# Performance work log

Measured on AMD Instinct MI355X. Metric: run time of the kernel, lower is better.

## Reference

```python
import jax, jax.numpy as jnp
import numpy as np

HEADS = 16
DIM_HEAD = 64
HEIGHT = 16
KERNEL = 5
DILATION = 1
ALPHA = 32 ** 2


def stable_softmax(t, axis=-1, alpha=ALPHA):
    t = t / alpha
    t = t - jax.lax.stop_gradient(jnp.max(t, axis=axis, keepdims=True))
    return jax.nn.softmax(t * alpha, axis=axis)


def setup_inputs() -> dict:
    key = jax.random.key(0)
    ks = jax.random.split(key, 5)
    b, n, dim = 4, 4097, 1024
    inner = HEADS * DIM_HEAD
    x = jax.random.normal(ks[0], (b, n, dim), dtype=jnp.float32)
    w_qkv = jax.random.normal(ks[1], (dim, 3 * inner), dtype=jnp.float32) * (dim ** -0.5)
    w_out = jax.random.normal(ks[2], (inner, dim), dtype=jnp.float32) * (inner ** -0.5)
    b_out = jax.random.normal(ks[3], (dim,), dtype=jnp.float32) * 0.02
    w_th = jax.random.normal(ks[4], (HEADS, HEADS), dtype=jnp.float32) * (HEADS ** -0.5)
    return {"x": x, "w_qkv": w_qkv, "w_out": w_out, "b_out": b_out, "w_th": w_th}


def reference(x, w_qkv, w_out, b_out, w_th):
    b, n, dim = x.shape
    h, d = HEADS, DIM_HEAD
    height, K, dil = HEIGHT, KERNEL, DILATION
    pad = dil * (K - 1) // 2
    scale = d ** -0.5
    kernel_numel = K * height

    # pad (n-1) non-BOS tokens to a multiple of height (static shapes)
    seq_pad = (-(n - 1)) % height
    xp = jnp.pad(x, ((0, 0), (0, seq_pad), (0, 0))) if seq_pad > 0 else x

    qkv = xp @ w_qkv  # [b, np, 3*inner]
    q, k, v = jnp.split(qkv, 3, axis=-1)

    if n == 1:  # bos-only path
        return v @ w_out + b_out

    out_bos = v[:, :1]  # [b, 1, inner]

    def to_heads(t):
        return t.reshape(b, -1, h, d).transpose(0, 2, 1, 3)  # [b,h,np,d]

    q, k, v = map(to_heads, (q, k, v))
    q = q * scale

    k_bos, k = k[:, :, 0], k[:, :, 1:]
    v_bos, v = v[:, :, 0], v[:, :, 1:]
    q = q[:, :, 1:]

    X = q.shape[2] // height  # number of timesteps

    # k, v as 2D grids [b,h,X,height,d]; unfold local windows along timestep axis
    k = k.reshape(b, h, X, height, d)
    v = v.reshape(b, h, X, height, d)
    kp = jnp.pad(k, ((0, 0), (0, 0), (pad, pad), (0, 0), (0, 0)))
    vp = jnp.pad(v, ((0, 0), (0, 0), (pad, pad), (0, 0), (0, 0)))
    idx = jnp.arange(X)[:, None] + jnp.arange(K)[None, :] * dil  # [X, K]
    kw = kp[:, :, idx].reshape(b, h, X, kernel_numel, d)  # [b,h,X,K*height,d]
    vw = vp[:, :, idx].reshape(b, h, X, kernel_numel, d)

    # prepend BOS key/value to every window
    kb = jnp.broadcast_to(k_bos[:, :, None, None, :], (b, h, X, 1, d))
    vb = jnp.broadcast_to(v_bos[:, :, None, None, :], (b, h, X, 1, d))
    kw = jnp.concatenate([kb, kw], axis=3)  # [b,h,X,1+kn,d]
    vw = jnp.concatenate([vb, vw], axis=3)

    qw = q.reshape(b, h, X, height, d)  # [b,h,X,height,d]
    sim = jnp.einsum('bhnid,bhnjd->bhnij', qw, kw)  # [b,h,X,height,1+kn]

    # causal mask over unfolded windows (BOS column never masked)
    seq_len = X * height
    q_range = jnp.arange(seq_len).reshape(X, height)
    k_range = jnp.pad(jnp.arange(seq_len).reshape(X, height), ((pad, pad), (0, 0)),
                      constant_values=seq_len)
    kr = k_range[idx].reshape(X, kernel_numel)  # [X, kn]
    mask = q_range[:, :, None] < kr[:, None, :]  # [X, height, kn]
    mask = jnp.pad(mask, ((0, 0), (0, 0), (1, 0)), constant_values=False)

    mask_value = -jnp.finfo(sim.dtype).max
    sim = jnp.where(mask[None, None], mask_value, sim)

    attn = stable_softmax(sim, axis=-1)
    # talking heads: 1x1x1 Conv3d over head channels == head mixing matmul
    attn = jnp.einsum('gh,bhnij->bgnij', w_th, attn)

    out = jnp.einsum('bhnij,bhnjd->bhnid', attn, vw)  # [b,h,X,height,d]
    out = out.transpose(0, 2, 3, 1, 4).reshape(b, X * height, h * d)
    out = jnp.concatenate([out_bos, out], axis=1)
    return (out @ w_out + b_out)[:, :n]
```

## Files before the change

kernel.cpp:

```cpp
#include <hip/hip_runtime.h>
#include <stdint.h>

typedef unsigned short u16;
typedef unsigned int u32;
typedef __attribute__((ext_vector_type(8))) short bf16x8;
typedef __attribute__((ext_vector_type(4))) float f32x4;

__device__ __forceinline__ float bf2f(u16 u) {
    union { u32 i; float f; } v; v.i = ((u32)u) << 16; return v.f;
}
__device__ __forceinline__ u16 f2bf(float f) {
    union { float f; u32 i; } v; v.f = f;
    u32 x = v.i;
    u32 r = (x + 0x7FFFu + ((x >> 16) & 1u)) >> 16;
    return (u16)r;
}

__device__ __forceinline__ void gld_lds16(const void* g, void* l) {
    __builtin_amdgcn_global_load_lds(
        (const __attribute__((address_space(1))) void*)g,
        (__attribute__((address_space(3))) void*)l, 16, 0, 0);
}

__global__ __launch_bounds__(256) void cvt_rows(
    const float* __restrict__ src, u16* __restrict__ dst, size_t total4) {
    size_t i = (size_t)blockIdx.x * 256 + threadIdx.x;
    if (i >= total4) return;
    const float4 v = ((const float4*)src)[i];
    u16 o[4] = {f2bf(v.x), f2bf(v.y), f2bf(v.z), f2bf(v.w)};
    *(unsigned long long*)(dst + i * 4) = *(unsigned long long*)o;
}

__global__ __launch_bounds__(256) void transpose_cvt(
    const float* __restrict__ src, u16* __restrict__ dst, int R, int C) {
    __shared__ float tile[32][33];
    int c0 = blockIdx.x * 32, r0 = blockIdx.y * 32;
    int tx = threadIdx.x & 31, ty = threadIdx.x >> 5;
    for (int rr = ty; rr < 32; rr += 8)
        tile[rr][tx] = src[(size_t)(r0 + rr) * C + c0 + tx];
    __syncthreads();
    for (int rr = ty; rr < 32; rr += 8)
        dst[(size_t)(c0 + rr) * R + r0 + tx] = f2bf(tile[tx][rr]);
}

template <int MODE>
__global__ __launch_bounds__(256, 2) void gemm_bt7(
    const u16* __restrict__ A, const u16* __restrict__ Bt,
    const float* __restrict__ bias, void* __restrict__ Cv,
    int M, int N, int K) {
    __shared__ u16 Asb[3][128 * 32];
    __shared__ u16 Bsb[3][256 * 32];
    int tid = threadIdx.x;
    int wid = tid >> 6, lane = tid & 63;
    int lr = lane & 15, lq = lane >> 4;
    int wr = wid >> 1, wc = wid & 1;
    int n0 = blockIdx.x * 256, m0 = blockIdx.y * 128;
    int NT = K >> 5;
    f32x4 acc[4][8] = {};

    #define ST_A(u, t, bi)                                                   \
    do {                                                                     \
        int g = (u) * 256 + tid;                                 \
        int row = g >> 2;                                        \
        int c = (g & 3) ^ ((row >> 1) & 3);                                  \
        int gm = m0 + row; if (gm >= M) gm = M - 1;                          \
        gld_lds16(A + (size_t)gm * K + ((t) << 5) + c * 8,                   \
                  &Asb[bi][g * 8]);                                          \
    } while (0)
    #define ST_B(u, t, bi)                                                   \
    do {                                                                     \
        int g = (u) * 256 + tid;                                \
        int row = g >> 2;                                        \
        int c = (g & 3) ^ ((row >> 1) & 3);                                  \
        gld_lds16(Bt + (size_t)(n0 + row) * K + ((t) << 5) + c * 8,          \
                  &Bsb[bi][g * 8]);                                          \
    } while (0)
    #define ST_TILE(t, bi)                                                   \
    do {                                                                     \
        ST_A(0, t, bi); ST_A(1, t, bi);                                      \
        ST_B(0, t, bi); ST_B(1, t, bi); ST_B(2, t, bi); ST_B(3, t, bi);      \
    } while (0)

    ST_TILE(0, 0);
    ST_TILE(1, 1);

    int bcur = 0;
    for (int t = 0; t < NT; ++t) {
        if (t + 1 < NT) asm volatile("s_waitcnt vmcnt(6)" ::: "memory");
        else            asm volatile("s_waitcnt vmcnt(0)" ::: "memory");
        asm volatile("s_barrier" ::: "memory");
        const u16* Ab = &Asb[bcur][0];
        const u16* Bb = &Bsb[bcur][0];
        bf16x8 a[4], b[8];
        #pragma unroll
        for (int mi = 0; mi < 4; ++mi) {
            int r = wr * 64 + mi * 16 + lr;
            int cs = lq ^ ((r >> 1) & 3);
            a[mi] = *(const bf16x8*)&Ab[r * 32 + cs * 8];
        }
        #pragma unroll
        for (int ni = 0; ni < 8; ++ni) {
            int r = wc * 128 + ni * 16 + lr;
            int cs = lq ^ ((r >> 1) & 3);
            b[ni] = *(const bf16x8*)&Bb[r * 32 + cs * 8];
        }
        if (t + 2 < NT) {
            int bst = bcur + 2; if (bst >= 3) bst -= 3;
            ST_TILE(t + 2, bst);
        }
        __builtin_amdgcn_s_setprio(1);
        #pragma unroll
        for (int mi = 0; mi < 4; ++mi)
            #pragma unroll
            for (int ni = 0; ni < 8; ++ni)
                acc[mi][ni] = __builtin_amdgcn_mfma_f32_16x16x32_bf16(
                    a[mi], b[ni], acc[mi][ni], 0, 0, 0);
        __builtin_amdgcn_s_setprio(0);
        bcur = bcur + 1; if (bcur == 3) bcur = 0;
    }
    #undef ST_A
    #undef ST_B
    #undef ST_TILE

    #pragma unroll
    for (int mi = 0; mi < 4; ++mi)
        #pragma unroll
        for (int ni = 0; ni < 8; ++ni) {
            int col = n0 + wc * 128 + ni * 16 + lr;
            float bv = (MODE == 1) ? bias[col] : 0.0f;
            #pragma unroll
            for (int r = 0; r < 4; ++r) {
                int row = m0 + wr * 64 + mi * 16 + lq * 4 + r;
                if (row < M) {
                    if (MODE == 0)
                        ((u16*)Cv)[(size_t)row * N + col] = f2bf(acc[mi][ni][r]);
                    else
                        ((float*)Cv)[(size_t)row * N + col] = acc[mi][ni][r] + bv;
                }
            }
        }
}

__global__ __launch_bounds__(256) void bos_copy(
    const u16* __restrict__ qkv, u16* __restrict__ attn_out) {
    int b = blockIdx.x;
    int c = blockIdx.y * 256 + threadIdx.x;
    attn_out[(size_t)b * 4097 * 1024 + c] =
        qkv[(size_t)b * 4097 * 3072 + 2048 + c];
}

__device__ __forceinline__ int pswz(int j, int i, int h) {
    int byte = j * 512 + i * 32 + h * 2;
    int sw = ((j & 7) ^ ((j >> 3) & 7) ^ ((i >> 2) & 3)) & 7;
    return byte ^ (sw << 4);
}

__global__ __launch_bounds__(512) void attn_kernel(
    const u16* __restrict__ qkv, const float* __restrict__ w_th,
    u16* __restrict__ attn_out) {
    __shared__ u16 P[64 * 16 * 16];
    __shared__ u16 vt[8][2048];

    int tid = threadIdx.x;
    int wid = tid >> 6, lane = tid & 63;
    int x = blockIdx.x;
    int b = blockIdx.y;
    size_t base = (size_t)b * 4097 * 3072;
    int lr = lane & 15;
    int lq = lane >> 4;
    int lk8 = lq * 8;

    bf16x8 bwth = {};
    if (lq < 2) {
        #pragma unroll
        for (int e = 0; e < 8; ++e)
            bwth[e] = (short)f2bf(w_th[lr * 16 + lk8 + e]);
    }

    for (int hh = 0; hh < 2; ++hh) {
        int h = wid * 2 + hh;
        const u16* qp = qkv + base + (size_t)(1 + x * 16 + lr) * 3072 + h * 64;
        bf16x8 aq0 = *(const bf16x8*)(qp + lk8);
        bf16x8 aq1 = *(const bf16x8*)(qp + 32 + lk8);
        f32x4 acc[4];
        #pragma unroll
        for (int jt = 0; jt < 4; ++jt) {
            int j = jt * 16 + lr;
            int tpos = x * 16 - 32 + (j - 1);
            int t = (j > 0 && tpos >= 0 && tpos < 4096) ? tpos + 1 : 0;
            const u16* kp = qkv + base + (size_t)t * 3072 + 1024 + h * 64;
            bf16x8 bk0 = *(const bf16x8*)(kp + lk8);
            bf16x8 bk1 = *(const bf16x8*)(kp + 32 + lk8);
            f32x4 c = {};
            c = __builtin_amdgcn_mfma_f32_16x16x32_bf16(aq0, bk0, c, 0, 0, 0);
            c = __builtin_amdgcn_mfma_f32_16x16x32_bf16(aq1, bk1, c, 0, 0, 0);
            acc[jt] = c;
        }
        float m[4], s[4], p[4][4];
        #pragma unroll
        for (int r = 0; r < 4; ++r) m[r] = -3.0e38f;
        #pragma unroll
        for (int jt = 0; jt < 4; ++jt) {
            int j = jt * 16 + lr;
            int tpos = x * 16 - 32 + (j - 1);
            bool jvalid = (j == 0) || (tpos >= 0);
            #pragma unroll
            for (int r = 0; r < 4; ++r) {
                int i = lq * 4 + r;
                bool keep = jvalid && (j == 0 || j <= i + 33);
                float v = keep ? acc[jt][r] * 0.125f : -3.0e38f;
                p[jt][r] = v;
                m[r] = fmaxf(m[r], v);
            }
        }
        #pragma unroll
        for (int r = 0; r < 4; ++r) {
            float v = m[r];
            v = fmaxf(v, __shfl_xor(v, 1));
            v = fmaxf(v, __shfl_xor(v, 2));
            v = fmaxf(v, __shfl_xor(v, 4));
            v = fmaxf(v, __shfl_xor(v, 8));
            m[r] = v; s[r] = 0.0f;
        }
        #pragma unroll
        for (int jt = 0; jt < 4; ++jt)
            #pragma unroll
            for (int r = 0; r < 4; ++r) {
                float e = __expf(p[jt][r] - m[r]);
                p[jt][r] = e; s[r] += e;
            }
        #pragma unroll
        for (int r = 0; r < 4; ++r) {
            float v = s[r];
            v += __shfl_xor(v, 1); v += __shfl_xor(v, 2);
            v += __shfl_xor(v, 4); v += __shfl_xor(v, 8);
            s[r] = 1.0f / v;
        }
        #pragma unroll
        for (int jt = 0; jt < 4; ++jt) {
            int j = jt * 16 + lr;
            #pragma unroll
            for (int r = 0; r < 4; ++r) {
                int i = lq * 4 + r;
                *(u16*)((char*)P + pswz(j, i, h)) = f2bf(p[jt][r] * s[r]);
            }
        }
    }
    __syncthreads();

    #pragma unroll
    for (int jj = 0; jj < 8; ++jj) {
        int j = wid * 8 + jj;
        bf16x8 a = {};
        if (lq < 2)
            a = *(const bf16x8*)((const char*)P + pswz(j, lr, lk8));
        f32x4 c = {};
        c = __builtin_amdgcn_mfma_f32_16x16x32_bf16(a, bwth, c, 0, 0, 0);
        #pragma unroll
        for (int r = 0; r < 4; ++r)
            *(u16*)((char*)P + pswz(j, lq * 4 + r, lr)) = f2bf(c[r]);
    }
    __syncthreads();

    const u16* vtw = &vt[wid][0];
    int jloc = lane >> 1, dh = lane & 1;
    for (int gg = 0; gg < 2; ++gg) {
        int g = wid * 2 + gg;
        f32x4 oacc[4] = {};
        #pragma unroll
        for (int kk = 0; kk < 2; ++kk) {
            {
                int jg = kk * 32 + jloc;
                int tpos = x * 16 - 32 + (jg - 1);
                int t = (jg > 0 && tpos >= 0 && tpos < 4096) ? tpos + 1 : 0;
                const u16* src = qkv + base + (size_t)t * 3072 + 2048 + g * 64
                               + dh * 8;
                #pragma unroll
                for (int w = 0; w < 4; ++w)
                    gld_lds16(src + w * 16, &vt[wid][w * 512 + lane * 8]);
            }
            bf16x8 av;
            #pragma unroll
            for (int e = 0; e < 8; ++e)
                av[e] = (short)*(const u16*)
                    ((const char*)P + pswz(kk * 32 + lk8 + e, lr, g));
            asm volatile("s_waitcnt vmcnt(0)" ::: "memory");
            #pragma unroll
            for (int dt = 0; dt < 4; ++dt) {
                bf16x8 bv;
                #pragma unroll
                for (int e = 0; e < 8; ++e)
                    bv[e] = (short)vtw[dt * 512 + (lk8 + e) * 16 + lr];
                oacc[dt] = __builtin_amdgcn_mfma_f32_16x16x32_bf16(
                    av, bv, oacc[dt], 0, 0, 0);
            }
        }
        #pragma unroll
        for (int dt = 0; dt < 4; ++dt) {
            int col = g * 64 + dt * 16 + lr;
            #pragma unroll
            for (int r = 0; r < 4; ++r) {
                int i = lq * 4 + r;
                size_t row = (size_t)b * 4097 + 1 + (size_t)x * 16 + i;
                attn_out[row * 1024 + col] = f2bf(oacc[dt][r]);
            }
        }
    }
}

extern "C" void kernel_launch(void* const* d_in, const int* in_sizes, int n_in,
                              void* d_out, int out_size, void* d_ws, size_t ws_size,
                              hipStream_t stream) {
    const float* x     = (const float*)d_in[0];
    const float* w_qkv = (const float*)d_in[1];
    const float* w_out = (const float*)d_in[2];
    const float* b_out = (const float*)d_in[3];
    const float* w_th  = (const float*)d_in[4];
    float* out = (float*)d_out;

    const int M = 4 * 4097;
    u16* qkv      = (u16*)d_ws;
    u16* wqkvT    = qkv + (size_t)M * 3072;
    u16* woutT    = wqkvT + (size_t)3072 * 1024;
    u16* xb       = woutT + (size_t)1024 * 1024;
    u16* attn_out = xb;

    transpose_cvt<<<dim3(96, 32), 256, 0, stream>>>(w_qkv, wqkvT, 1024, 3072);
    transpose_cvt<<<dim3(32, 32), 256, 0, stream>>>(w_out, woutT, 1024, 1024);

    size_t total4 = (size_t)M * 1024 / 4;
    cvt_rows<<<(int)((total4 + 255) / 256), 256, 0, stream>>>(x, xb, total4);

    int mt = (M + 127) / 128;
    gemm_bt7<0><<<dim3(3072 / 256, mt), 256, 0, stream>>>(
        xb, wqkvT, nullptr, qkv, M, 3072, 1024);

    bos_copy<<<dim3(4, 4), 256, 0, stream>>>(qkv, attn_out);
    attn_kernel<<<dim3(256, 4), 512, 0, stream>>>(qkv, w_th, attn_out);

    gemm_bt7<1><<<dim3(1024 / 256, mt), 256, 0, stream>>>(
        attn_out, woutT, b_out, out, M, 1024, 1024);
}
```

Baseline: 271.5 us.

## Double-buffer V tile loads into LDS and swizzle to avoid bank conflicts

Measured after the change: 274.5 us. About the same (+1.1%).

```diff
diff --git a/kernel.cpp b/kernel.cpp
--- a/kernel.cpp
+++ b/kernel.cpp
@@ -159,7 +159,7 @@
     const u16* __restrict__ qkv, const float* __restrict__ w_th,
     u16* __restrict__ attn_out) {
     __shared__ u16 P[64 * 16 * 16];
-    __shared__ u16 vt[8][2048];
+    __shared__ u16 vt[8][2][512];
 
     int tid = threadIdx.x;
     int wid = tid >> 6, lane = tid & 63;
@@ -262,39 +262,53 @@
     }
     __syncthreads();
 
-    const u16* vtw = &vt[wid][0];
-    int jloc = lane >> 1, dh = lane & 1;
-    for (int gg = 0; gg < 2; ++gg) {
-        int g = wid * 2 + gg;
-        f32x4 oacc[4] = {};
-        #pragma unroll
-        for (int kk = 0; kk < 2; ++kk) {
-            {
-                int jg = kk * 32 + jloc;
-                int tpos = x * 16 - 32 + (jg - 1);
-                int t = (jg > 0 && tpos >= 0 && tpos < 4096) ? tpos + 1 : 0;
-                const u16* src = qkv + base + (size_t)t * 3072 + 2048 + g * 64
-                               + dh * 8;
-                #pragma unroll
-                for (int w = 0; w < 4; ++w)
-                    gld_lds16(src + w * 16, &vt[wid][w * 512 + lane * 8]);
-            }
-            bf16x8 av;
+    int jl = lane >> 1;
+    int dsw = ((lane & 1) ^ ((jl >> 3) & 1)) * 8;
+    int drd = lr ^ ((lq & 1) * 8);
+    f32x4 oacc[2][4] = {};
+    bf16x8 av;
+
+    #define AISSUE(u)                                                        \
+    do {                                                                     \
+        int hh_ = (u) >> 3, kk_ = ((u) >> 2) & 1, dt_ = (u) & 3;             \
+        int g_ = wid * 2 + hh_;                                              \
+        int jg = kk_ * 32 + jl;                                              \
+        int tpos = x * 16 - 32 + (jg - 1);                                   \
+        int t_ = (jg > 0 && tpos >= 0 && tpos < 4096) ? tpos + 1 : 0;        \
+        gld_lds16(qkv + base + (size_t)t_ * 3072 + 2048 + g_ * 64            \
+                  + dt_ * 16 + dsw,                                          \
+                  &vt[wid][(u) & 1][lane * 8]);                              \
+    } while (0)
+
+    AISSUE(0);
+    #pragma unroll
+    for (int u = 0; u < 16; ++u) {
+        if (u < 15) {
+            asm volatile("" ::: "memory");
+            AISSUE(u + 1);
+        }
+        if ((u & 3) == 0) {
+            int g = wid * 2 + (u >> 3);
+            int kk = (u >> 2) & 1;
             #pragma unroll
             for (int e = 0; e < 8; ++e)
                 av[e] = (short)*(const u16*)
                     ((const char*)P + pswz(kk * 32 + lk8 + e, lr, g));
-            asm volatile("s_waitcnt vmcnt(0)" ::: "memory");
-            #pragma unroll
-            for (int dt = 0; dt < 4; ++dt) {
-                bf16x8 bv;
-                #pragma unroll
-                for (int e = 0; e < 8; ++e)
-                    bv[e] = (short)vtw[dt * 512 + (lk8 + e) * 16 + lr];
-                oacc[dt] = __builtin_amdgcn_mfma_f32_16x16x32_bf16(
-                    av, bv, oacc[dt], 0, 0, 0);
-            }
-        }
+        }
+        if (u < 15) asm volatile("s_waitcnt vmcnt(1)" ::: "memory");
+        else        asm volatile("s_waitcnt vmcnt(0)" ::: "memory");
+        bf16x8 bv;
+        #pragma unroll
+        for (int e = 0; e < 8; ++e)
+            bv[e] = (short)vt[wid][u & 1][(lk8 + e) * 16 + drd];
+        oacc[u >> 3][u & 3] = __builtin_amdgcn_mfma_f32_16x16x32_bf16(
+            av, bv, oacc[u >> 3][u & 3], 0, 0, 0);
+    }
+    #undef AISSUE
+
+    #pragma unroll
+    for (int hh = 0; hh < 2; ++hh) {
+        int g = wid * 2 + hh;
         #pragma unroll
         for (int dt = 0; dt < 4; ++dt) {
             int col = g * 64 + dt * 16 + lr;
@@ -302,7 +316,7 @@
             for (int r = 0; r < 4; ++r) {
                 int i = lq * 4 + r;
                 size_t row = (size_t)b * 4097 + 1 + (size_t)x * 16 + i;
-                attn_out[row * 1024 + col] = f2bf(oacc[dt][r]);
+                attn_out[row * 1024 + col] = f2bf(oacc[hh][dt][r]);
             }
         }
     }
```
